# Kernel tuning notes

Hardware: AMD Instinct MI355X
Metric: run time of the kernel (lower is better)

## Reference

```python
import jax, jax.numpy as jnp
import numpy as np

D_MODEL = 1024
NUM_HEADS = 16
D_K = D_MODEL // NUM_HEADS  # 64
MAX_SEQ_LEN = 2048
THETA = 10000.0
BATCH = 2
SEQ = 2048


def _rope_tables():
    # freqs: [d_k/2], positions: [max_seq_len] -> angles [max_seq_len, d_k/2]
    freqs = THETA ** (-jnp.arange(0, D_K, 2, dtype=jnp.float32) / D_K)
    positions = jnp.arange(MAX_SEQ_LEN, dtype=jnp.float32)[:, None]
    angles = positions * freqs[None, :]
    return jnp.cos(angles), jnp.sin(angles)


def _apply_rope(x, token_positions, cos_cached, sin_cached):
    # x: [..., seq, d_k]; token_positions: [seq]
    cos = cos_cached[token_positions]  # [seq, d_k/2]
    sin = sin_cached[token_positions]
    x_even = x[..., ::2]
    x_odd = x[..., 1::2]
    r_even = x_even * cos - x_odd * sin
    r_odd = x_even * sin + x_odd * cos
    # interleave even/odd back into last dim
    out = jnp.stack([r_even, r_odd], axis=-1)
    return out.reshape(x.shape)


def setup_inputs() -> dict:
    key = jax.random.key(0)
    ks = jax.random.split(key, 5)
    scale = 1.0 / np.sqrt(D_MODEL)
    in_features = jax.random.normal(ks[0], (BATCH, SEQ, D_MODEL), dtype=jnp.float32)
    q_proj = jax.random.normal(ks[1], (D_MODEL, D_MODEL), dtype=jnp.float32) * scale
    k_proj = jax.random.normal(ks[2], (D_MODEL, D_MODEL), dtype=jnp.float32) * scale
    v_proj = jax.random.normal(ks[3], (D_MODEL, D_MODEL), dtype=jnp.float32) * scale
    o_proj = jax.random.normal(ks[4], (D_MODEL, D_MODEL), dtype=jnp.float32) * scale
    mask = jnp.tril(jnp.ones((SEQ, SEQ), dtype=bool))  # causal
    token_positions = jnp.arange(SEQ, dtype=jnp.int32)
    return {
        "in_features": in_features,
        "q_proj": q_proj,
        "k_proj": k_proj,
        "v_proj": v_proj,
        "o_proj": o_proj,
        "mask": mask,
        "token_positions": token_positions,
    }


def reference(in_features, q_proj, k_proj, v_proj, o_proj, mask, token_positions):
    B, S, _ = in_features.shape
    cos_cached, sin_cached = _rope_tables()
    # fused QKV projection (same math as x @ cat(Wq,Wk,Wv).T then chunk)
    q = jnp.einsum("bsd,ed->bse", in_features, q_proj)
    k = jnp.einsum("bsd,ed->bse", in_features, k_proj)
    v = jnp.einsum("bsd,ed->bse", in_features, v_proj)
    # ... seq (h d) -> ... h seq d
    q = q.reshape(B, S, NUM_HEADS, D_K).transpose(0, 2, 1, 3)
    k = k.reshape(B, S, NUM_HEADS, D_K).transpose(0, 2, 1, 3)
    v = v.reshape(B, S, NUM_HEADS, D_K).transpose(0, 2, 1, 3)
    q = _apply_rope(q, token_positions, cos_cached, sin_cached)
    k = _apply_rope(k, token_positions, cos_cached, sin_cached)
    scores = jnp.einsum("bhqd,bhkd->bhqk", q, k) / np.sqrt(D_K)
    scores = jnp.where(mask, scores, -jnp.inf)
    attn = jax.nn.softmax(scores, axis=-1)
    out = jnp.einsum("bhqk,bhkd->bhqd", attn, v)
    # ... h seq d -> ... seq (h d)
    concat = out.transpose(0, 2, 1, 3).reshape(B, S, D_MODEL)
    return jnp.einsum("bsd,ed->bse", concat, o_proj)
```

## Files before the change

### kernel.cpp

```cpp
#include <hip/hip_runtime.h>
#include <cstdint>

#define D_MODEL 1024
#define NHEADS 16
#define DKH 64
#define SEQL 2048
#define NBATCH 2
#define NROWS (NBATCH * SEQL)

typedef __bf16 bf16;
typedef __bf16 bf16x2 __attribute__((ext_vector_type(2)));
typedef __bf16 bf16x4 __attribute__((ext_vector_type(4)));
typedef __bf16 bf16x8 __attribute__((ext_vector_type(8)));
typedef float f32x4 __attribute__((ext_vector_type(4)));
typedef float f32x16 __attribute__((ext_vector_type(16)));
typedef unsigned u32x4 __attribute__((ext_vector_type(4)));

static __device__ __forceinline__ f32x4 mfma16(bf16x8 a, bf16x8 b, f32x4 c) {
  return __builtin_amdgcn_mfma_f32_16x16x32_bf16(a, b, c, 0, 0, 0);
}

static __device__ __forceinline__ f32x16 mfma32(bf16x8 a, bf16x8 b, f32x16 c) {
  return __builtin_amdgcn_mfma_f32_32x32x16_bf16(a, b, c, 0, 0, 0);
}

static __device__ __forceinline__ void gload_lds16(const bf16* g, bf16* l) {
  __builtin_amdgcn_global_load_lds(
      (const __attribute__((address_space(1))) void*)g,
      (__attribute__((address_space(3))) void*)l, 16, 0, 0);
}

static __device__ __forceinline__ float fexp2(float x) {
  return __builtin_amdgcn_exp2f(x);
}

static __device__ __forceinline__ unsigned cvt_pk(float a, float b) {
  unsigned r;
  asm("v_cvt_pk_bf16_f32 %0, %1, %2" : "=v"(r) : "v"(a), "v"(b));
  return r;
}

static __device__ __forceinline__ void plswap(unsigned& a, unsigned& b) {
  asm("v_permlane32_swap_b32 %0, %1" : "+v"(a), "+v"(b));
}

__global__ __launch_bounds__(256) void convert_kernel(
    const float* __restrict__ x, const float* __restrict__ wq,
    const float* __restrict__ wk, const float* __restrict__ wv,
    const float* __restrict__ wo, bf16* __restrict__ xb,
    bf16* __restrict__ wqb, bf16* __restrict__ wkb, bf16* __restrict__ wvb,
    bf16* __restrict__ wob) {
  int i4 = blockIdx.x * 256 + threadIdx.x;
  const float* src;
  bf16* dst;
  int off;
  if (i4 < (NROWS * D_MODEL / 4)) {
    src = x; dst = xb; off = i4;
  } else {
    int j = i4 - NROWS * D_MODEL / 4;
    int sel = j >> 18;
    off = j & ((1 << 18) - 1);
    src = sel == 0 ? wq : sel == 1 ? wk : sel == 2 ? wv : wo;
    dst = sel == 0 ? wqb : sel == 1 ? wkb : sel == 2 ? wvb : wob;
  }
  float4 v = ((const float4*)src)[off];
  bf16x4 o;
  o[0] = (bf16)v.x; o[1] = (bf16)v.y; o[2] = (bf16)v.z; o[3] = (bf16)v.w;
  ((bf16x4*)dst)[off] = o;
}

__global__ __launch_bounds__(256, 3) void qkv_gemm(
    const bf16* __restrict__ A, const bf16* __restrict__ Bq,
    const bf16* __restrict__ Bk, const bf16* __restrict__ Bv,
    const int* __restrict__ tpos, bf16* __restrict__ Qb,
    bf16* __restrict__ Kb, bf16* __restrict__ Vt) {
  __shared__ bf16 As[128 * 64];
  __shared__ bf16 Bs[3][64 * 64];
  const int t = threadIdx.x, wave = t >> 6, lane = t & 63;
  const int quad = lane >> 4, l16 = lane & 15;
  const int bm = blockIdx.x * 128, bn = blockIdx.y * 64;

  f32x4 acc[3][2][4];
  for (int o = 0; o < 3; o++)
    for (int mt = 0; mt < 2; mt++)
      for (int nt = 0; nt < 4; nt++)
        for (int r = 0; r < 4; r++) acc[o][mt][nt][r] = 0.0f;

  for (int k0 = 0; k0 < D_MODEL; k0 += 64) {
    for (int j = 0; j < 4; j++) {
      int s = (wave * 4 + j) * 64 + lane;
      int srow = s >> 3, scol = (s & 7) ^ (srow & 7);
      gload_lds16(&A[(size_t)(bm + srow) * D_MODEL + k0 + scol * 8],
                  &As[(wave * 4 + j) * 512]);
    }
    for (int j = 0; j < 2; j++) {
      int s = (wave * 2 + j) * 64 + lane;
      int srow = s >> 3, scol = (s & 7) ^ (srow & 7);
      size_t goff = (size_t)(bn + srow) * D_MODEL + k0 + scol * 8;
      gload_lds16(&Bq[goff], &Bs[0][(wave * 2 + j) * 512]);
      gload_lds16(&Bk[goff], &Bs[1][(wave * 2 + j) * 512]);
      gload_lds16(&Bv[goff], &Bs[2][(wave * 2 + j) * 512]);
    }
    __syncthreads();
    for (int kh = 0; kh < 2; kh++) {
      const int kc = kh * 4 + quad;
      bf16x8 af[2];
      for (int mt = 0; mt < 2; mt++) {
        int row = wave * 32 + mt * 16 + l16;
        af[mt] = *(bf16x8*)&As[row * 64 + (kc ^ (row & 7)) * 8];
      }
      for (int nt = 0; nt < 4; nt++) {
        int row = nt * 16 + l16;
        int off = row * 64 + (kc ^ (row & 7)) * 8;
        bf16x8 bq = *(bf16x8*)&Bs[0][off];
        bf16x8 bk = *(bf16x8*)&Bs[1][off];
        bf16x8 bv = *(bf16x8*)&Bs[2][off];
        for (int mt = 0; mt < 2; mt++) {
          acc[0][mt][nt] = mfma16(af[mt], bq, acc[0][mt][nt]);
          acc[1][mt][nt] = mfma16(af[mt], bk, acc[1][mt][nt]);
          acc[2][mt][nt] = mfma16(af[mt], bv, acc[2][mt][nt]);
        }
      }
    }
    __syncthreads();
  }

  const float qsc = 0.125f * 1.44269504f;
  float freqv[4], sgn[4];
  for (int nt = 0; nt < 4; nt++) {
    int cp = (bn + nt * 16 + l16) & 63;
    freqv[nt] = fexp2((float)(cp >> 1) * -0.41524101f);
    sgn[nt] = (cp & 1) ? 1.0f : -1.0f;
  }
  for (int mt = 0; mt < 2; mt++) {
    int row0 = bm + wave * 32 + mt * 16 + quad * 4;
    for (int r = 0; r < 4; r++) {
      int row = row0 + r;
      float pos = (float)tpos[row & (SEQL - 1)];
      for (int nt = 0; nt < 4; nt++) {
        int col = bn + nt * 16 + l16;
        float sn, cs;
        __sincosf(pos * freqv[nt], &sn, &cs);
        float vq = acc[0][mt][nt][r];
        float vk = acc[1][mt][nt][r];
        float pq = __shfl_xor(vq, 1);
        float pk = __shfl_xor(vk, 1);
        float rq = vq * cs + sgn[nt] * pq * sn;
        float rk = vk * cs + sgn[nt] * pk * sn;
        Qb[(size_t)row * D_MODEL + col] = (bf16)(rq * qsc);
        Kb[(size_t)row * D_MODEL + col] = (bf16)rk;
      }
    }
    for (int nt = 0; nt < 4; nt++) {
      int col = bn + nt * 16 + l16;
      bf16x4 pv;
      for (int r = 0; r < 4; r++) pv[r] = (bf16)acc[2][mt][nt][r];
      *(bf16x4*)&Vt[(size_t)col * NROWS + row0] = pv;
    }
  }
}

template <int BM, int BN, typename OutT>
__device__ __forceinline__ void gemm_body64(const bf16* __restrict__ A,
                                            const bf16* __restrict__ Bm,
                                            OutT* __restrict__ C, int bm,
                                            int bn, int N, int K) {
  constexpr int MT = BM / 32, NT = BN / 32;
  constexpr int CA = BM / 32, CB = BN / 32;
  __shared__ bf16 As[BM * 64];
  __shared__ bf16 Bs[BN * 64];
  const int t = threadIdx.x;
  const int wave = t >> 6, lane = t & 63;
  const int quad = lane >> 4, l16 = lane & 15;
  const int wm = (wave >> 1) * (MT * 16), wn = (wave & 1) * (NT * 16);

  f32x4 acc[MT][NT];
  for (int i = 0; i < MT; i++)
    for (int j = 0; j < NT; j++)
      for (int r = 0; r < 4; r++) acc[i][j][r] = 0.0f;

  for (int k0 = 0; k0 < K; k0 += 64) {
    for (int j = 0; j < CA; j++) {
      int s = (wave * CA + j) * 64 + lane;
      int srow = s >> 3, scol = (s & 7) ^ (srow & 7);
      gload_lds16(&A[(size_t)(bm + srow) * K + k0 + scol * 8],
                  &As[(wave * CA + j) * 512]);
    }
    for (int j = 0; j < CB; j++) {
      int s = (wave * CB + j) * 64 + lane;
      int srow = s >> 3, scol = (s & 7) ^ (srow & 7);
      gload_lds16(&Bm[(size_t)(bn + srow) * K + k0 + scol * 8],
                  &Bs[(wave * CB + j) * 512]);
    }
    __syncthreads();
    for (int kh = 0; kh < 2; kh++) {
      const int kc = kh * 4 + quad;
      bf16x8 af[MT], bfr[NT];
      for (int mt = 0; mt < MT; mt++) {
        int row = wm + mt * 16 + l16;
        af[mt] = *(bf16x8*)&As[row * 64 + (kc ^ (row & 7)) * 8];
      }
      for (int nt = 0; nt < NT; nt++) {
        int row = wn + nt * 16 + l16;
        bfr[nt] = *(bf16x8*)&Bs[row * 64 + (kc ^ (row & 7)) * 8];
      }
      for (int mt = 0; mt < MT; mt++)
        for (int nt = 0; nt < NT; nt++)
          acc[mt][nt] = mfma16(af[mt], bfr[nt], acc[mt][nt]);
    }
    __syncthreads();
  }
  for (int mt = 0; mt < MT; mt++)
    for (int nt = 0; nt < NT; nt++)
      for (int r = 0; r < 4; r++) {
        int row = bm + wm + mt * 16 + quad * 4 + r;
        int col = bn + wn + nt * 16 + l16;
        C[(size_t)row * N + col] = (OutT)acc[mt][nt][r];
      }
}

__global__ __launch_bounds__(256, 3) void o_gemm(const bf16* __restrict__ A,
                                                 const bf16* __restrict__ Bm,
                                                 float* __restrict__ C) {
  gemm_body64<64, 128, float>(A, Bm, C, blockIdx.x * 64, blockIdx.y * 128,
                              D_MODEL, D_MODEL);
}

__global__ __launch_bounds__(256) void attn_kernel(
    const bf16* __restrict__ Q, const bf16* __restrict__ K,
    const bf16* __restrict__ Vt_g, float* __restrict__ O0,
    float* __restrict__ O1, float* __restrict__ O2, float* __restrict__ O3,
    float* __restrict__ L0, float* __restrict__ L1, float* __restrict__ L2,
    float* __restrict__ L3) {
  const int t = threadIdx.x;
  const int wave = t >> 6, lane = t & 63;
  const int l32 = lane & 31, hi = lane >> 5;

  const int id = blockIdx.x;
  const int bh = id & 31;
  const int c = 39 - (id >> 5);
  int qt, piece, np;
  if (c < 4)       { qt = c;                 piece = 0;            np = 1; }
  else if (c < 12) { int e = c - 4;  qt = 4 + (e >> 1); piece = e & 1; np = 2; }
  else if (c < 24) { int e = c - 12; qt = 8 + e / 3;    piece = e % 3; np = 3; }
  else             { int e = c - 24; qt = 12 + (e >> 2); piece = e & 3; np = 4; }
  const int total = qt + 1, bas = total / np, rem = total % np;
  const int len = bas + (piece < rem ? 1 : 0);
  const int k0 = piece * bas + (piece < rem ? piece : rem);

  const int b = bh >> 4, h = bh & 15;
  const int q_base = qt * 128;
  const size_t base = (size_t)b * SEQL * D_MODEL + h * DKH;

  __shared__ bf16 lds[16384];

  const int r8 = lane >> 3, c8 = lane & 7;

  for (int i = 0; i < 4; i++) {
    int row = wave * 32 + i * 8 + r8;
    int sc = c8 ^ (row & 7);
    gload_lds16(&Q[base + (size_t)(q_base + row) * D_MODEL + sc * 8],
                &lds[(wave * 32 + i * 8) * 64]);
  }
  __syncthreads();
  bf16x8 qb[4];
  {
    int row = wave * 32 + l32;
#pragma unroll
    for (int ks = 0; ks < 4; ks++) {
      int ch = (ks * 2 + hi) ^ (row & 7);
      qb[ks] = *(bf16x8*)&lds[row * 64 + ch * 8];
    }
  }
  __syncthreads();

  f32x16 oaccT[2];
  float lsum = 0.0f;
#pragma unroll
  for (int dt = 0; dt < 2; dt++)
#pragma unroll
    for (int r = 0; r < 16; r++) oaccT[dt][r] = 0.0f;

  const bf16* Vrow0 = &Vt_g[(size_t)(h * 64) * NROWS + b * SEQL];
  const int q_glob = q_base + wave * 32 + l32;

  auto stage = [&](int hc) {
    int buf = hc & 1;
    int kb = k0 * 128 + hc * 64;
#pragma unroll
    for (int i = 0; i < 2; i++) {
      int seg = wave * 2 + i;
      int row = seg * 8 + r8;
      int sc = c8 ^ (row & 7);
      gload_lds16(&K[base + (size_t)(kb + row) * D_MODEL + sc * 8],
                  &lds[buf * 4096 + seg * 512]);
      gload_lds16(&Vrow0[(size_t)row * NROWS + kb + sc * 8],
                  &lds[8192 + buf * 4096 + seg * 512]);
    }
  };

  const int nch = 2 * len;
  stage(0);
  for (int hc = 0; hc < nch; hc++) {
    if (hc + 1 < nch) {
      stage(hc + 1);
      asm volatile("s_waitcnt vmcnt(4)" ::: "memory");
    } else {
      asm volatile("s_waitcnt vmcnt(0)" ::: "memory");
    }
    __builtin_amdgcn_sched_barrier(0);
    __builtin_amdgcn_s_barrier();

    const int buf = hc & 1;
    const bf16* Kb_ = &lds[buf * 4096];
    const bf16* Vb_ = &lds[8192 + buf * 4096];
    const int kb = k0 * 128 + hc * 64;
    const bool diag = ((kb >> 7) == qt);

#pragma unroll
    for (int cc = 0; cc < 2; cc++) {
      f32x16 sT;
#pragma unroll
      for (int r = 0; r < 16; r++) sT[r] = 0.0f;
      {
        int krow = cc * 32 + l32;
#pragma unroll
        for (int ks = 0; ks < 4; ks++) {
          int ch = (ks * 2 + hi) ^ (krow & 7);
          bf16x8 kf = *(bf16x8*)&Kb_[krow * 64 + ch * 8];
          sT = mfma32(kf, qb[ks], sT);
        }
      }
      if (diag) {
#pragma unroll
        for (int r = 0; r < 16; r++) {
          int key = kb + cc * 32 + (r & 3) + 8 * (r >> 2) + 4 * hi;
          if (key > q_glob) sT[r] = -1e30f;
        }
      }
      float p[16];
#pragma unroll
      for (int r = 0; r < 16; r++) p[r] = fexp2(sT[r]);
      lsum += (((p[0] + p[1]) + (p[2] + p[3])) +
               ((p[4] + p[5]) + (p[6] + p[7]))) +
              (((p[8] + p[9]) + (p[10] + p[11])) +
               ((p[12] + p[13]) + (p[14] + p[15])));
      unsigned a0 = cvt_pk(p[0], p[1]),  a1 = cvt_pk(p[2], p[3]);
      unsigned b0 = cvt_pk(p[4], p[5]),  b1 = cvt_pk(p[6], p[7]);
      unsigned c0 = cvt_pk(p[8], p[9]),  c1 = cvt_pk(p[10], p[11]);
      unsigned d0 = cvt_pk(p[12], p[13]), d1 = cvt_pk(p[14], p[15]);
      plswap(a0, b0); plswap(a1, b1); plswap(c0, d0); plswap(c1, d1);
      bf16x8 pf[2];
      {
        u32x4 u = {a0, a1, b0, b1};
        pf[0] = __builtin_bit_cast(bf16x8, u);
      }
      {
        u32x4 u = {c0, c1, d0, d1};
        pf[1] = __builtin_bit_cast(bf16x8, u);
      }
#pragma unroll
      for (int dt = 0; dt < 2; dt++) {
        int d = dt * 32 + l32;
#pragma unroll
        for (int ks = 0; ks < 2; ks++) {
          int ch = (cc * 4 + ks * 2 + hi) ^ (d & 7);
          bf16x8 vf = *(bf16x8*)&Vb_[d * 64 + ch * 8];
          oaccT[dt] = mfma32(vf, pf[ks], oaccT[dt]);
        }
      }
    }
    asm volatile("" ::: "memory");
    __builtin_amdgcn_sched_barrier(0);
    __builtin_amdgcn_s_barrier();
  }

  lsum += __shfl_xor(lsum, 32);
  float* Ob;
  float* Lb;
  int rbase, roff;
  if (piece == 0)      { Ob = O0; Lb = L0; rbase = SEQL;        roff = 0; }
  else if (piece == 1) { Ob = O1; Lb = L1; rbase = SEQL - 512;  roff = 512; }
  else if (piece == 2) { Ob = O2; Lb = L2; rbase = SEQL - 1024; roff = 1024; }
  else                 { Ob = O3; Lb = L3; rbase = SEQL - 1536; roff = 1536; }
  {
    int qrow = q_base + wave * 32 + l32;
    size_t orow = (size_t)b * rbase + (qrow - roff);
    if (hi == 0) Lb[orow * NHEADS + h] = lsum;
#pragma unroll
    for (int dt = 0; dt < 2; dt++)
#pragma unroll
      for (int rq = 0; rq < 4; rq++) {
        f32x4 vv = {oaccT[dt][rq * 4 + 0], oaccT[dt][rq * 4 + 1],
                    oaccT[dt][rq * 4 + 2], oaccT[dt][rq * 4 + 3]};
        *(f32x4*)&Ob[orow * D_MODEL + h * DKH + dt * 32 + rq * 8 + hi * 4] =
            vv;
      }
  }
}

__global__ __launch_bounds__(256) void normalize_kernel(
    const float* __restrict__ O0, const float* __restrict__ O1,
    const float* __restrict__ O2, const float* __restrict__ O3,
    const float* __restrict__ L0, const float* __restrict__ L1,
    const float* __restrict__ L2, const float* __restrict__ L3,
    bf16* __restrict__ Cc) {
  int i4 = blockIdx.x * 256 + threadIdx.x;
  int row = i4 >> 8;
  int c0 = (i4 & 255) * 4;
  int s = row & (SEQL - 1);
  int b = row >> 11;
  int h = c0 >> 6;
  float l = L0[(size_t)row * NHEADS + h];
  f32x4 v = *(const f32x4*)&O0[(size_t)row * D_MODEL + c0];
  if (s >= 512) {
    size_t r1 = (size_t)b * (SEQL - 512) + (s - 512);
    l += L1[r1 * NHEADS + h];
    f32x4 u = *(const f32x4*)&O1[r1 * D_MODEL + c0];
    for (int r = 0; r < 4; r++) v[r] += u[r];
  }
  if (s >= 1024) {
    size_t r2 = (size_t)b * (SEQL - 1024) + (s - 1024);
    l += L2[r2 * NHEADS + h];
    f32x4 u = *(const f32x4*)&O2[r2 * D_MODEL + c0];
    for (int r = 0; r < 4; r++) v[r] += u[r];
  }
  if (s >= 1536) {
    size_t r3 = (size_t)b * (SEQL - 1536) + (s - 1536);
    l += L3[r3 * NHEADS + h];
    f32x4 u = *(const f32x4*)&O3[r3 * D_MODEL + c0];
    for (int r = 0; r < 4; r++) v[r] += u[r];
  }
  float inv = 1.0f / l;
  bf16x4 o;
  o[0] = (bf16)(v[0] * inv);
  o[1] = (bf16)(v[1] * inv);
  o[2] = (bf16)(v[2] * inv);
  o[3] = (bf16)(v[3] * inv);
  *(bf16x4*)&Cc[(size_t)row * D_MODEL + c0] = o;
}

extern "C" void kernel_launch(void* const* d_in, const int* in_sizes, int n_in,
                              void* d_out, int out_size, void* d_ws,
                              size_t ws_size, hipStream_t stream) {
  const float* x = (const float*)d_in[0];
  const float* wq = (const float*)d_in[1];
  const float* wk = (const float*)d_in[2];
  const float* wv = (const float*)d_in[3];
  const float* wo = (const float*)d_in[4];
  const int* tpos = (const int*)d_in[6];
  float* out = (float*)d_out;

  char* p = (char*)d_ws;
  bf16* xb  = (bf16*)p; p += (size_t)NROWS * D_MODEL * 2;
  bf16* wqb = (bf16*)p; p += (size_t)D_MODEL * D_MODEL * 2;
  bf16* wkb = (bf16*)p; p += (size_t)D_MODEL * D_MODEL * 2;
  bf16* wvb = (bf16*)p; p += (size_t)D_MODEL * D_MODEL * 2;
  bf16* wob = (bf16*)p; p += (size_t)D_MODEL * D_MODEL * 2;
  bf16* Qb  = (bf16*)p; p += (size_t)NROWS * D_MODEL * 2;
  bf16* Kb  = (bf16*)p; p += (size_t)NROWS * D_MODEL * 2;
  bf16* Vt  = (bf16*)p; p += (size_t)NROWS * D_MODEL * 2;
  bf16* Cc  = (bf16*)p; p += (size_t)NROWS * D_MODEL * 2;
  float* O0 = (float*)p; p += (size_t)NROWS * D_MODEL * 4;
  float* L0 = (float*)p; p += (size_t)NROWS * NHEADS * 4;
  float* O1 = (float*)p; p += (size_t)NBATCH * (SEQL - 512) * D_MODEL * 4;
  float* L1 = (float*)p; p += (size_t)NBATCH * (SEQL - 512) * NHEADS * 4;
  float* O2 = (float*)xb;
  float* O3 = (float*)wqb;
  float* L2 = (float*)wvb;
  float* L3 = (float*)wvb + (size_t)NBATCH * (SEQL - 1024) * NHEADS;

  convert_kernel<<<8192, 256, 0, stream>>>(x, wq, wk, wv, wo, xb, wqb, wkb,
                                           wvb, wob);
  qkv_gemm<<<dim3(NROWS / 128, D_MODEL / 64), 256, 0, stream>>>(
      xb, wqb, wkb, wvb, tpos, Qb, Kb, Vt);
  attn_kernel<<<1280, 256, 0, stream>>>(Qb, Kb, Vt, O0, O1, O2, O3, L0, L1,
                                        L2, L3);
  normalize_kernel<<<NROWS * D_MODEL / 1024, 256, 0, stream>>>(
      O0, O1, O2, O3, L0, L1, L2, L3, Cc);
  o_gemm<<<dim3(NROWS / 64, D_MODEL / 128), 256, 0, stream>>>(Cc, wob, out);
}
```

Baseline: 184.2 us.

## Fuse split-KV combine and normalization into the output projection GEMM prologue

```diff
diff --git a/kernel.cpp b/kernel.cpp
--- a/kernel.cpp
+++ b/kernel.cpp
@@ -160,70 +160,96 @@
   }
 }
 
-template <int BM, int BN, typename OutT>
-__device__ __forceinline__ void gemm_body64(const bf16* __restrict__ A,
-                                            const bf16* __restrict__ Bm,
-                                            OutT* __restrict__ C, int bm,
-                                            int bn, int N, int K) {
-  constexpr int MT = BM / 32, NT = BN / 32;
-  constexpr int CA = BM / 32, CB = BN / 32;
-  __shared__ bf16 As[BM * 64];
-  __shared__ bf16 Bs[BN * 64];
+__global__ __launch_bounds__(256, 3) void og_norm(
+    const float* __restrict__ O0, const float* __restrict__ O1,
+    const float* __restrict__ O2, const float* __restrict__ O3,
+    const float* __restrict__ L0, const float* __restrict__ L1,
+    const float* __restrict__ L2, const float* __restrict__ L3,
+    const bf16* __restrict__ Bm, float* __restrict__ C) {
+  constexpr int MT = 2, NT = 4;
+  const int bm = blockIdx.x * 64, bn = blockIdx.y * 128;
+  __shared__ bf16 As[64 * 64];
+  __shared__ bf16 Bs[128 * 64];
   const int t = threadIdx.x;
   const int wave = t >> 6, lane = t & 63;
   const int quad = lane >> 4, l16 = lane & 15;
-  const int wm = (wave >> 1) * (MT * 16), wn = (wave & 1) * (NT * 16);
+  const int wm = (wave >> 1) * 32, wn = (wave & 1) * 64;
+  const int tr = t >> 4, tc = t & 15;
 
   f32x4 acc[MT][NT];
   for (int i = 0; i < MT; i++)
     for (int j = 0; j < NT; j++)
       for (int r = 0; r < 4; r++) acc[i][j][r] = 0.0f;
 
-  for (int k0 = 0; k0 < K; k0 += 64) {
-    for (int j = 0; j < CA; j++) {
-      int s = (wave * CA + j) * 64 + lane;
+  for (int kt = 0; kt < 16; kt++) {
+    __syncthreads();
+#pragma unroll
+    for (int j = 0; j < 4; j++) {
+      int s = (wave * 4 + j) * 64 + lane;
       int srow = s >> 3, scol = (s & 7) ^ (srow & 7);
-      gload_lds16(&A[(size_t)(bm + srow) * K + k0 + scol * 8],
-                  &As[(wave * CA + j) * 512]);
-    }
-    for (int j = 0; j < CB; j++) {
-      int s = (wave * CB + j) * 64 + lane;
-      int srow = s >> 3, scol = (s & 7) ^ (srow & 7);
-      gload_lds16(&Bm[(size_t)(bn + srow) * K + k0 + scol * 8],
-                  &Bs[(wave * CB + j) * 512]);
+      gload_lds16(&Bm[(size_t)(bn + srow) * D_MODEL + kt * 64 + scol * 8],
+                  &Bs[(wave * 4 + j) * 512]);
+    }
+    const int h = kt;
+#pragma unroll
+    for (int rr = 0; rr < 4; rr++) {
+      int rl = tr + rr * 16;
+      int grow = bm + rl;
+      int s = grow & (SEQL - 1), b = grow >> 11;
+      float l = L0[(size_t)grow * NHEADS + h];
+      f32x4 v = *(const f32x4*)&O0[(size_t)grow * D_MODEL + kt * 64 + tc * 4];
+      if (s >= 512) {
+        size_t r1 = (size_t)b * (SEQL - 512) + (s - 512);
+        l += L1[r1 * NHEADS + h];
+        f32x4 u = *(const f32x4*)&O1[r1 * D_MODEL + kt * 64 + tc * 4];
+        for (int r = 0; r < 4; r++) v[r] += u[r];
+      }
+      if (s >= 1024) {
+        size_t r2 = (size_t)b * (SEQL - 1024) + (s - 1024);
+        l += L2[r2 * NHEADS + h];
+        f32x4 u = *(const f32x4*)&O2[r2 * D_MODEL + kt * 64 + tc * 4];
+        for (int r = 0; r < 4; r++) v[r] += u[r];
+      }
+      if (s >= 1536) {
+        size_t r3 = (size_t)b * (SEQL - 1536) + (s - 1536);
+        l += L3[r3 * NHEADS + h];
+        f32x4 u = *(const f32x4*)&O3[r3 * D_MODEL + kt * 64 + tc * 4];
+        for (int r = 0; r < 4; r++) v[r] += u[r];
+      }
+      float inv = 1.0f / l;
+      bf16x4 o;
+      for (int r = 0; r < 4; r++) o[r] = (bf16)(v[r] * inv);
+      *(bf16x4*)&As[rl * 64 + ((tc >> 1) ^ (rl & 7)) * 8 + (tc & 1) * 4] = o;
     }
     __syncthreads();
+#pragma unroll
     for (int kh = 0; kh < 2; kh++) {
       const int kc = kh * 4 + quad;
       bf16x8 af[MT], bfr[NT];
+#pragma unroll
       for (int mt = 0; mt < MT; mt++) {
         int row = wm + mt * 16 + l16;
         af[mt] = *(bf16x8*)&As[row * 64 + (kc ^ (row & 7)) * 8];
       }
+#pragma unroll
       for (int nt = 0; nt < NT; nt++) {
         int row = wn + nt * 16 + l16;
         bfr[nt] = *(bf16x8*)&Bs[row * 64 + (kc ^ (row & 7)) * 8];
       }
+#pragma unroll
       for (int mt = 0; mt < MT; mt++)
+#pragma unroll
         for (int nt = 0; nt < NT; nt++)
           acc[mt][nt] = mfma16(af[mt], bfr[nt], acc[mt][nt]);
     }
-    __syncthreads();
   }
   for (int mt = 0; mt < MT; mt++)
     for (int nt = 0; nt < NT; nt++)
       for (int r = 0; r < 4; r++) {
         int row = bm + wm + mt * 16 + quad * 4 + r;
         int col = bn + wn + nt * 16 + l16;
-        C[(size_t)row * N + col] = (OutT)acc[mt][nt][r];
-      }
-}
-
-__global__ __launch_bounds__(256, 3) void o_gemm(const bf16* __restrict__ A,
-                                                 const bf16* __restrict__ Bm,
-                                                 float* __restrict__ C) {
-  gemm_body64<64, 128, float>(A, Bm, C, blockIdx.x * 64, blockIdx.y * 128,
-                              D_MODEL, D_MODEL);
+        C[(size_t)row * D_MODEL + col] = acc[mt][nt][r];
+      }
 }
 
 __global__ __launch_bounds__(256) void attn_kernel(
@@ -397,47 +423,6 @@
             vv;
       }
   }
-}
-
-__global__ __launch_bounds__(256) void normalize_kernel(
-    const float* __restrict__ O0, const float* __restrict__ O1,
-    const float* __restrict__ O2, const float* __restrict__ O3,
-    const float* __restrict__ L0, const float* __restrict__ L1,
-    const float* __restrict__ L2, const float* __restrict__ L3,
-    bf16* __restrict__ Cc) {
-  int i4 = blockIdx.x * 256 + threadIdx.x;
-  int row = i4 >> 8;
-  int c0 = (i4 & 255) * 4;
-  int s = row & (SEQL - 1);
-  int b = row >> 11;
-  int h = c0 >> 6;
-  float l = L0[(size_t)row * NHEADS + h];
-  f32x4 v = *(const f32x4*)&O0[(size_t)row * D_MODEL + c0];
-  if (s >= 512) {
-    size_t r1 = (size_t)b * (SEQL - 512) + (s - 512);
-    l += L1[r1 * NHEADS + h];
-    f32x4 u = *(const f32x4*)&O1[r1 * D_MODEL + c0];
-    for (int r = 0; r < 4; r++) v[r] += u[r];
-  }
-  if (s >= 1024) {
-    size_t r2 = (size_t)b * (SEQL - 1024) + (s - 1024);
-    l += L2[r2 * NHEADS + h];
-    f32x4 u = *(const f32x4*)&O2[r2 * D_MODEL + c0];
-    for (int r = 0; r < 4; r++) v[r] += u[r];
-  }
-  if (s >= 1536) {
-    size_t r3 = (size_t)b * (SEQL - 1536) + (s - 1536);
-    l += L3[r3 * NHEADS + h];
-    f32x4 u = *(const f32x4*)&O3[r3 * D_MODEL + c0];
-    for (int r = 0; r < 4; r++) v[r] += u[r];
-  }
-  float inv = 1.0f / l;
-  bf16x4 o;
-  o[0] = (bf16)(v[0] * inv);
-  o[1] = (bf16)(v[1] * inv);
-  o[2] = (bf16)(v[2] * inv);
-  o[3] = (bf16)(v[3] * inv);
-  *(bf16x4*)&Cc[(size_t)row * D_MODEL + c0] = o;
 }
 
 extern "C" void kernel_launch(void* const* d_in, const int* in_sizes, int n_in,
@@ -469,6 +454,7 @@
   float* O3 = (float*)wqb;
   float* L2 = (float*)wvb;
   float* L3 = (float*)wvb + (size_t)NBATCH * (SEQL - 1024) * NHEADS;
+  (void)Cc;
 
   convert_kernel<<<8192, 256, 0, stream>>>(x, wq, wk, wv, wo, xb, wqb, wkb,
                                            wvb, wob);
@@ -476,7 +462,6 @@
       xb, wqb, wkb, wvb, tpos, Qb, Kb, Vt);
   attn_kernel<<<1280, 256, 0, stream>>>(Qb, Kb, Vt, O0, O1, O2, O3, L0, L1,
                                         L2, L3);
-  normalize_kernel<<<NROWS * D_MODEL / 1024, 256, 0, stream>>>(
-      O0, O1, O2, O3, L0, L1, L2, L3, Cc);
-  o_gemm<<<dim3(NROWS / 64, D_MODEL / 128), 256, 0, stream>>>(Cc, wob, out);
-}
+  og_norm<<<dim3(NROWS / 64, D_MODEL / 128), 256, 0, stream>>>(
+      O0, O1, O2, O3, L0, L1, L2, L3, wob, out);
+}
```

Measured after the change: 260.8 us. +41.6%, slower.
